# Performance work log

Hardware: AMD Instinct MI355X
Metric: run time of the kernel (lower is better)

Reference implementation:

```python
import jax, jax.numpy as jnp
import numpy as np

B, N, C, H = 4, 128, 512, 8
D = C // H
SCALE = D ** (-0.5) * 50.0


def setup_inputs() -> dict:
    key = jax.random.key(0)
    kx, kw = jax.random.split(key)
    x = jax.random.normal(kx, (B, N, N, C), dtype=jnp.float32)
    # torch Linear(n_embd, 5*n_embd, bias=False); stored here as [in, out] for x @ w
    w_qkv = jax.random.normal(kw, (C, 5 * C), dtype=jnp.float32) * (C ** -0.5)
    return {"x": x, "w_qkv": w_qkv}


def _heads(t):
    # [b, i, j, h*d] -> [b, h, i, j, d]
    b, i, j, _ = t.shape
    return t.reshape(b, i, j, H, D).transpose(0, 3, 1, 2, 4)


def reference(x, w_qkv):
    # global norm over the entire tensor (torch .std() is unbiased, ddof=1)
    x = (x - x.mean()) / x.std(ddof=1)
    qkv = x @ w_qkv                                   # [b, i, j, 5c]
    q, k1, k2, v1, v2 = map(_heads, jnp.split(qkv, 5, axis=-1))
    # pivotal attention: for query (i,j), pivot over k with row stream k1[i,k]
    # and column stream k2[k,j]
    scores = SCALE * (jnp.einsum('bhijd,bhikd->bhijk', q, k1)
                      + jnp.einsum('bhijd,bhkjd->bhijk', q, k2))
    attn = jax.nn.softmax(scores, axis=-1)            # [b, h, i, j, k]
    out = (jnp.einsum('bhijk,bhikd->bhijd', attn, v1)
           + jnp.einsum('bhijk,bhkjd->bhijd', attn, v2))
    # [b, h, i, j, d] -> [b, i, j, h*d]
    return out.transpose(0, 2, 3, 1, 4).reshape(B, N, N, C)
```

## Files before the change

kernel.cpp:

```cpp
#include <hip/hip_runtime.h>
#include <stdint.h>


typedef __attribute__((ext_vector_type(8))) short s8v;
typedef __attribute__((ext_vector_type(4))) float f4v;

#define MFMA(a, b, c) __builtin_amdgcn_mfma_f32_16x16x32_bf16((a), (b), (c), 0, 0, 0)

__device__ __forceinline__ float bf2f(unsigned short u) {
  union { unsigned int i; float f; } v; v.i = ((unsigned int)u) << 16; return v.f;
}
__device__ __forceinline__ unsigned short f2bf(float f) {
  union { float f; unsigned int i; } v; v.f = f;
  unsigned int i = v.i;
  return (unsigned short)((i + 0x7fffu + ((i >> 16) & 1u)) >> 16);
}

__device__ __forceinline__ void async_copy16(const void* g, void* l) {
  __builtin_amdgcn_global_load_lds(
      (const __attribute__((address_space(1))) unsigned int*)(uintptr_t)g,
      (__attribute__((address_space(3))) unsigned int*)(uintptr_t)l,
      16, 0, 0);
}

__global__ __launch_bounds__(256) void k_probe(const unsigned short* __restrict__ x,
                                               int* __restrict__ flag) {
  uint4 v = ((const uint4*)x)[threadIdx.x];
  unsigned int uu[4] = {v.x, v.y, v.z, v.w};
  int bad = 0;
#pragma unroll
  for (int u = 0; u < 4; ++u) {
    float a = bf2f((unsigned short)(uu[u] & 0xffffu));
    float b = bf2f((unsigned short)(uu[u] >> 16));
    if (!(fabsf(a) <= 1e4f)) bad = 1;
    if (!(fabsf(b) <= 1e4f)) bad = 1;
  }
  if (bad) atomicOr(flag, 1);
}

__global__ __launch_bounds__(256) void k_red(const void* __restrict__ xraw,
                                             const int* __restrict__ flag,
                                             double* __restrict__ dstats) {
  __shared__ float red[8];
  const int fm = flag[0];
  int t = threadIdx.x;
  size_t gid = (size_t)blockIdx.x * 256 + t;
  float s = 0.f, ss = 0.f;
  if (fm) {
    const float4* pf = (const float4*)xraw;
#pragma unroll 4
    for (int it = 0; it < 32; ++it) {
      size_t idx = gid + (size_t)it * 131072;
      float4 u1 = pf[2 * idx], u2 = pf[2 * idx + 1];
      float vals[8] = {u1.x, u1.y, u1.z, u1.w, u2.x, u2.y, u2.z, u2.w};
#pragma unroll
      for (int u = 0; u < 8; ++u) { s += vals[u]; ss += vals[u] * vals[u]; }
    }
  } else {
    const uint4* p = (const uint4*)xraw;
#pragma unroll 4
    for (int it = 0; it < 32; ++it) {
      uint4 v = p[gid + (size_t)it * 131072];
      unsigned int uu[4] = {v.x, v.y, v.z, v.w};
#pragma unroll
      for (int u = 0; u < 4; ++u) {
        float a = bf2f((unsigned short)(uu[u] & 0xffffu));
        float b = bf2f((unsigned short)(uu[u] >> 16));
        s += a + b;
        ss += a * a + b * b;
      }
    }
  }
#pragma unroll
  for (int d = 32; d >= 1; d >>= 1) {
    s += __shfl_down(s, d);
    ss += __shfl_down(ss, d);
  }
  int lane = t & 63, wave = t >> 6;
  if (lane == 0) { red[wave] = s; red[4 + wave] = ss; }
  __syncthreads();
  if (t == 0) {
    atomicAdd(&dstats[0], (double)(red[0] + red[1] + red[2] + red[3]));
    atomicAdd(&dstats[1], (double)(red[4] + red[5] + red[6] + red[7]));
  }
}

__global__ void k_stats(const double* __restrict__ dstats, float* __restrict__ fstats) {
  double M = 33554432.0;
  double mean = dstats[0] / M;
  double var = (dstats[1] - dstats[0] * dstats[0] / M) / (M - 1.0);
  double istd = 1.0 / sqrt(var);
  fstats[0] = (float)istd;
  fstats[1] = (float)(-mean * istd);
}

__global__ __launch_bounds__(256) void k_colsum(const void* __restrict__ wraw,
                                                const int* __restrict__ flag,
                                                float* __restrict__ colsum) {
  const int fm = flag[0];
  int c = blockIdx.x * 256 + threadIdx.x;
  if (c >= 2560) return;
  float s = 0.f;
  if (fm) {
    const float* w = (const float*)wraw;
    for (int r = 0; r < 512; ++r) s += w[(size_t)r * 2560 + c];
  } else {
    const unsigned short* w = (const unsigned short*)wraw;
    for (int r = 0; r < 512; ++r) s += bf2f(w[(size_t)r * 2560 + c]);
  }
  colsum[c] = s;
}

__global__ __launch_bounds__(256) void k_wt(const void* __restrict__ wraw,
                                            const int* __restrict__ flag,
                                            unsigned short* __restrict__ wThi,
                                            unsigned short* __restrict__ wTlo) {
  __shared__ float tile[64][65];
  const int fm = flag[0];
  int n0 = blockIdx.x * 64, r0 = blockIdx.y * 64;
#pragma unroll
  for (int rep = 0; rep < 16; ++rep) {
    int idx = rep * 256 + threadIdx.x;
    int r = idx >> 6, n = idx & 63;
    float v;
    if (fm) v = ((const float*)wraw)[(size_t)(r0 + r) * 2560 + n0 + n];
    else    v = bf2f(((const unsigned short*)wraw)[(size_t)(r0 + r) * 2560 + n0 + n]);
    tile[r][n] = v;
  }
  __syncthreads();
#pragma unroll
  for (int rep = 0; rep < 16; ++rep) {
    int idx = rep * 256 + threadIdx.x;
    int n = idx >> 6, r = idx & 63;
    float v = tile[r][n];
    unsigned short hi = f2bf(v);
    size_t o = (size_t)(n0 + n) * 512 + r0 + r;
    wThi[o] = hi;
    wTlo[o] = f2bf(v - bf2f(hi));
  }
}

__global__ __launch_bounds__(256) void k_convx(const void* __restrict__ xraw,
                                               const int* __restrict__ flag,
                                               unsigned short* __restrict__ xhi,
                                               unsigned short* __restrict__ xlo,
                                               int b) {
  const int fm = flag[0];
  size_t e0 = ((size_t)blockIdx.x * 256 + threadIdx.x) * 8;
  size_t g0 = (size_t)b * 8388608 + e0;
  float vals[8];
  if (fm) {
    const float4* pf = (const float4*)xraw;
    float4 u1 = pf[g0 / 4], u2 = pf[g0 / 4 + 1];
    vals[0] = u1.x; vals[1] = u1.y; vals[2] = u1.z; vals[3] = u1.w;
    vals[4] = u2.x; vals[5] = u2.y; vals[6] = u2.z; vals[7] = u2.w;
  } else {
    uint4 v = ((const uint4*)xraw)[g0 / 8];
    unsigned int uu[4] = {v.x, v.y, v.z, v.w};
#pragma unroll
    for (int u = 0; u < 4; ++u) {
      vals[2 * u] = bf2f((unsigned short)(uu[u] & 0xffffu));
      vals[2 * u + 1] = bf2f((unsigned short)(uu[u] >> 16));
    }
  }
  unsigned short h[8], l[8];
#pragma unroll
  for (int u = 0; u < 8; ++u) {
    h[u] = f2bf(vals[u]);
    l[u] = f2bf(vals[u] - bf2f(h[u]));
  }
  *(uint4*)(xhi + e0) = *(const uint4*)h;
  *(uint4*)(xlo + e0) = *(const uint4*)l;
}

__global__ __launch_bounds__(256) void k_gemm(
    const unsigned short* __restrict__ xhi, const unsigned short* __restrict__ xlo,
    const unsigned short* __restrict__ wThi, const unsigned short* __restrict__ wTlo,
    const float* __restrict__ colsum, const float* __restrict__ fstats,
    const int* __restrict__ flag,
    unsigned short* __restrict__ qhi, unsigned short* __restrict__ qlo,
    unsigned short* __restrict__ k1hi, unsigned short* __restrict__ k1lo,
    unsigned short* __restrict__ k2hi, unsigned short* __restrict__ k2lo,
    unsigned short* __restrict__ v1T, unsigned short* __restrict__ v2d,
    int h0, int hcShift, int nwgy) {
  __shared__ __align__(16) unsigned short Ash[2][4096];
  __shared__ __align__(16) unsigned short Asl[2][4096];
  __shared__ __align__(16) unsigned short Bsh[2][4096];
  __shared__ __align__(16) unsigned short Bsl[2][4096];
  const int fm = flag[0];
  const int t = threadIdx.x;

  const int vid = blockIdx.x;
  const int xcd = vid & 7, seq = vid >> 3;
  const int m0 = (xcd * 16 + seq / nwgy) * 128;
  const int n0 = (seq % nwgy) * 128;

  const int hcMask = (1 << hcShift) - 1;

  const int lane = t & 63, wave = t >> 6;
  const int wm = (wave & 1) * 64, wn = (wave >> 1) * 64;
  const int l16 = lane & 15, q4 = lane >> 4;

  const int srow0 = t >> 2;
  const int srow1 = 64 + srow0;
  const int sch = (((t & 3) ^ ((t >> 3) & 3)) << 3);
  const int swoff = ((q4 ^ ((l16 >> 1) & 3)) << 3);

  const float af = fstats[0], bfc = fstats[1];
  const unsigned short* xh = xhi + (size_t)m0 * 512;
  const unsigned short* xl = xlo + (size_t)m0 * 512;

  int wcol0, wcol1;
  {
    int n = n0 + srow0, g = n >> hcShift, rem = n & hcMask;
    wcol0 = (g << 9) + ((h0 + (rem >> 6)) << 6) + (rem & 63);
    n = n0 + srow1; g = n >> hcShift; rem = n & hcMask;
    wcol1 = (g << 9) + ((h0 + (rem >> 6)) << 6) + (rem & 63);
  }

  f4v acc[4][4];
#pragma unroll
  for (int a = 0; a < 4; ++a)
#pragma unroll
    for (int c = 0; c < 4; ++c) acc[a][c] = (f4v)0.f;

  auto STAGE = [&](int bsel, int k0) {
    async_copy16(xh + (size_t)srow0 * 512 + k0 + sch, (char*)&Ash[bsel][0] + t * 16);
    async_copy16(xh + (size_t)srow1 * 512 + k0 + sch, (char*)&Ash[bsel][0] + (256 + t) * 16);
    async_copy16(wThi + (size_t)wcol0 * 512 + k0 + sch, (char*)&Bsh[bsel][0] + t * 16);
    async_copy16(wThi + (size_t)wcol1 * 512 + k0 + sch, (char*)&Bsh[bsel][0] + (256 + t) * 16);
    if (fm) {
      async_copy16(xl + (size_t)srow0 * 512 + k0 + sch, (char*)&Asl[bsel][0] + t * 16);
      async_copy16(xl + (size_t)srow1 * 512 + k0 + sch, (char*)&Asl[bsel][0] + (256 + t) * 16);
      async_copy16(wTlo + (size_t)wcol0 * 512 + k0 + sch, (char*)&Bsl[bsel][0] + t * 16);
      async_copy16(wTlo + (size_t)wcol1 * 512 + k0 + sch, (char*)&Bsl[bsel][0] + (256 + t) * 16);
    }
  };

  STAGE(0, 0);

#pragma unroll 2
  for (int ks = 0; ks < 16; ++ks) {
    const int kb = ks & 1;
    if (ks < 15) {
      STAGE(kb ^ 1, (ks + 1) << 5);
      if (fm) asm volatile("s_waitcnt vmcnt(8)" ::: "memory");
      else    asm volatile("s_waitcnt vmcnt(4)" ::: "memory");
    } else {
      asm volatile("s_waitcnt vmcnt(0)" ::: "memory");
    }
    __builtin_amdgcn_s_barrier();

    s8v ah[4], bh[4];
#pragma unroll
    for (int jt = 0; jt < 4; ++jt)
      ah[jt] = *(const s8v*)&Ash[kb][(wm + jt * 16 + l16) * 32 + swoff];
#pragma unroll
    for (int nt = 0; nt < 4; ++nt)
      bh[nt] = *(const s8v*)&Bsh[kb][(wn + nt * 16 + l16) * 32 + swoff];
    if (fm) {
      s8v al[4], bl[4];
#pragma unroll
      for (int jt = 0; jt < 4; ++jt)
        al[jt] = *(const s8v*)&Asl[kb][(wm + jt * 16 + l16) * 32 + swoff];
#pragma unroll
      for (int nt = 0; nt < 4; ++nt)
        bl[nt] = *(const s8v*)&Bsl[kb][(wn + nt * 16 + l16) * 32 + swoff];
#pragma unroll
      for (int jt = 0; jt < 4; ++jt)
#pragma unroll
        for (int nt = 0; nt < 4; ++nt) {
          acc[jt][nt] = MFMA(ah[jt], bh[nt], acc[jt][nt]);
          acc[jt][nt] = MFMA(ah[jt], bl[nt], acc[jt][nt]);
          acc[jt][nt] = MFMA(al[jt], bh[nt], acc[jt][nt]);
        }
    } else {
#pragma unroll
      for (int jt = 0; jt < 4; ++jt)
#pragma unroll
        for (int nt = 0; nt < 4; ++nt) acc[jt][nt] = MFMA(ah[jt], bh[nt], acc[jt][nt]);
    }
    asm volatile("" ::: "memory");
    __builtin_amdgcn_s_barrier();
  }

#pragma unroll
  for (int jt = 0; jt < 4; ++jt) {
#pragma unroll
    for (int nt = 0; nt < 4; ++nt) {
      int gcol = n0 + wn + nt * 16 + l16;
      int g = gcol >> hcShift, rem = gcol & hcMask;
      int hl = rem >> 6, d = rem & 63;
      int wcol = (g << 9) + ((h0 + hl) << 6) + d;
      float cs = colsum[wcol] * bfc;
#pragma unroll
      for (int r = 0; r < 4; ++r) {
        int grow = m0 + wm + jt * 16 + q4 * 4 + r;
        int i = grow >> 7, j = grow & 127;
        float val = acc[jt][nt][r] * af + cs;
        unsigned short hi = f2bf(val);
        if (g == 0) {
          size_t idx = (((size_t)hl * 128 + i) * 128 + j) * 64 + d;
          qhi[idx] = hi; qlo[idx] = f2bf(val - bf2f(hi));
        } else if (g == 1) {
          size_t idx = (((size_t)hl * 128 + i) * 128 + j) * 64 + d;
          k1hi[idx] = hi; k1lo[idx] = f2bf(val - bf2f(hi));
        } else if (g == 2) {
          size_t idx = (((size_t)hl * 128 + j) * 128 + i) * 64 + d;
          k2hi[idx] = hi; k2lo[idx] = f2bf(val - bf2f(hi));
        } else if (g == 3) {
          size_t idx = (((size_t)hl * 128 + i) * 64 + d) * 128 + j;
          v1T[idx] = hi;
        } else {
          size_t idx = (((size_t)hl * 128 + i) * 128 + j) * 64 + d;
          v2d[idx] = hi;
        }
      }
    }
  }
}

__global__ __launch_bounds__(256) void k_v2t(const unsigned short* __restrict__ v2d,
                                             unsigned short* __restrict__ v2T) {
  __shared__ unsigned short T[128][72];
  const int j = blockIdx.x, hl = blockIdx.y;
  const int t = threadIdx.x;
  const unsigned short* ib = v2d + ((size_t)hl * 128) * 8192 + (size_t)j * 64;
#pragma unroll
  for (int it = 0; it < 4; ++it) {
    int c = it * 256 + t;
    int p = c >> 3, d8 = (c & 7) * 8;
    uint4 v = *(const uint4*)(ib + (size_t)p * 8192 + d8);
    *(uint4*)&T[p][d8 ^ (((p >> 3) & 7) << 3)] = v;
  }
  __syncthreads();
  unsigned short* ob = v2T + (((size_t)hl * 128 + j) * 64) * 128;
#pragma unroll
  for (int it = 0; it < 4; ++it) {
    int c = it * 256 + t;
    int d = c >> 4, p8 = (c & 15) * 8;
    int dz = d ^ (((p8 >> 3) & 7) << 3);
    unsigned short u[8];
#pragma unroll
    for (int e = 0; e < 8; ++e) u[e] = T[p8 + e][dz];
    *(uint4*)&ob[(size_t)d * 128 + p8] = *(const uint4*)u;
  }
}

__global__ __launch_bounds__(256) void k_s1(
    const unsigned short* __restrict__ qhi, const unsigned short* __restrict__ qlo,
    const unsigned short* __restrict__ k1hi, const unsigned short* __restrict__ k1lo,
    float* __restrict__ S) {
  const int i = blockIdx.x, hl = blockIdx.y;
  const int t = threadIdx.x, lane = t & 63, wave = t >> 6;
  const int l16 = lane & 15, q4 = lane >> 4;
  const size_t base = ((size_t)hl * 128 + i) * 128 * 64;

  f4v acc[2][8];
#pragma unroll
  for (int a = 0; a < 2; ++a)
#pragma unroll
    for (int c = 0; c < 8; ++c) acc[a][c] = (f4v)0.f;

#pragma unroll
  for (int kc = 0; kc < 2; ++kc) {
    s8v ah[2], al[2];
#pragma unroll
    for (int jt = 0; jt < 2; ++jt) {
      size_t off = base + (size_t)(wave * 32 + jt * 16 + l16) * 64 + kc * 32 + q4 * 8;
      ah[jt] = *(const s8v*)(qhi + off);
      al[jt] = *(const s8v*)(qlo + off);
    }
#pragma unroll
    for (int kt = 0; kt < 8; ++kt) {
      size_t off = base + (size_t)(kt * 16 + l16) * 64 + kc * 32 + q4 * 8;
      s8v bh = *(const s8v*)(k1hi + off);
      s8v bl = *(const s8v*)(k1lo + off);
#pragma unroll
      for (int jt = 0; jt < 2; ++jt) {
        acc[jt][kt] = MFMA(ah[jt], bh, acc[jt][kt]);
        acc[jt][kt] = MFMA(ah[jt], bl, acc[jt][kt]);
        acc[jt][kt] = MFMA(al[jt], bh, acc[jt][kt]);
      }
    }
  }
  float* Sb = S + ((size_t)hl * 128 + i) * 128 * 128;
#pragma unroll
  for (int jt = 0; jt < 2; ++jt)
#pragma unroll
    for (int kt = 0; kt < 8; ++kt)
#pragma unroll
      for (int r = 0; r < 4; ++r) {
        int j = wave * 32 + jt * 16 + q4 * 4 + r;
        Sb[(size_t)j * 128 + kt * 16 + l16] = acc[jt][kt][r];
      }
}

__global__ __launch_bounds__(256) void k_s2(
    const unsigned short* __restrict__ qhi, const unsigned short* __restrict__ qlo,
    const unsigned short* __restrict__ k2hi, const unsigned short* __restrict__ k2lo,
    const float* __restrict__ S, unsigned short* __restrict__ attn) {
  const int j = blockIdx.x, hl = blockIdx.y;
  const int t = threadIdx.x, lane = t & 63, wave = t >> 6;
  const int l16 = lane & 15, q4 = lane >> 4;
  const size_t bbase = ((size_t)hl * 128 + j) * 128 * 64;

  f4v acc[2][8];
#pragma unroll
  for (int a = 0; a < 2; ++a)
#pragma unroll
    for (int c = 0; c < 8; ++c) acc[a][c] = (f4v)0.f;

#pragma unroll
  for (int kc = 0; kc < 2; ++kc) {
    s8v ah[2], al[2];
#pragma unroll
    for (int it = 0; it < 2; ++it) {
      size_t off = (((size_t)hl * 128 + (wave * 32 + it * 16 + l16)) * 128 + j) * 64 +
                   kc * 32 + q4 * 8;
      ah[it] = *(const s8v*)(qhi + off);
      al[it] = *(const s8v*)(qlo + off);
    }
#pragma unroll
    for (int kt = 0; kt < 8; ++kt) {
      size_t off = bbase + (size_t)(kt * 16 + l16) * 64 + kc * 32 + q4 * 8;
      s8v bh = *(const s8v*)(k2hi + off);
      s8v bl = *(const s8v*)(k2lo + off);
#pragma unroll
      for (int it = 0; it < 2; ++it) {
        acc[it][kt] = MFMA(ah[it], bh, acc[it][kt]);
        acc[it][kt] = MFMA(ah[it], bl, acc[it][kt]);
        acc[it][kt] = MFMA(al[it], bh, acc[it][kt]);
      }
    }
  }

#pragma unroll
  for (int it = 0; it < 2; ++it) {
#pragma unroll
    for (int r = 0; r < 4; ++r) {
      int i = wave * 32 + it * 16 + q4 * 4 + r;
      const float* Srow = S + (((size_t)hl * 128 + i) * 128 + j) * 128;
      float tv[8];
      float m = -3.4e38f;
#pragma unroll
      for (int kt = 0; kt < 8; ++kt) {
        tv[kt] = 6.25f * (Srow[kt * 16 + l16] + acc[it][kt][r]);
        m = fmaxf(m, tv[kt]);
      }
#pragma unroll
      for (int d = 1; d <= 8; d <<= 1) m = fmaxf(m, __shfl_xor(m, d));
      float sum = 0.f;
#pragma unroll
      for (int kt = 0; kt < 8; ++kt) {
        tv[kt] = __expf(tv[kt] - m);
        sum += tv[kt];
      }
#pragma unroll
      for (int d = 1; d <= 8; d <<= 1) sum += __shfl_xor(sum, d);
      float rs = 1.f / sum;
      unsigned short* arow = attn + (((size_t)hl * 128 + i) * 128 + j) * 128;
#pragma unroll
      for (int kt = 0; kt < 8; ++kt) arow[kt * 16 + l16] = f2bf(tv[kt] * rs);
    }
  }
}

__global__ __launch_bounds__(256) void k_av1(
    const unsigned short* __restrict__ attn, const unsigned short* __restrict__ v1T,
    unsigned short* __restrict__ out1) {
  const int i = blockIdx.x, hl = blockIdx.y;
  const int t = threadIdx.x, lane = t & 63, wave = t >> 6;
  const int l16 = lane & 15, q4 = lane >> 4;
  const size_t abase = ((size_t)hl * 128 + i) * 128 * 128;
  const size_t vbase = ((size_t)hl * 128 + i) * 64 * 128;

  f4v acc[2][4];
#pragma unroll
  for (int a = 0; a < 2; ++a)
#pragma unroll
    for (int c = 0; c < 4; ++c) acc[a][c] = (f4v)0.f;

#pragma unroll
  for (int kc = 0; kc < 4; ++kc) {
    s8v a[2], bfr[4];
#pragma unroll
    for (int jt = 0; jt < 2; ++jt)
      a[jt] = *(const s8v*)(attn + abase + (size_t)(wave * 32 + jt * 16 + l16) * 128 +
                            kc * 32 + q4 * 8);
#pragma unroll
    for (int dt = 0; dt < 4; ++dt)
      bfr[dt] = *(const s8v*)(v1T + vbase + (size_t)(dt * 16 + l16) * 128 + kc * 32 + q4 * 8);
#pragma unroll
    for (int jt = 0; jt < 2; ++jt)
#pragma unroll
      for (int dt = 0; dt < 4; ++dt) acc[jt][dt] = MFMA(a[jt], bfr[dt], acc[jt][dt]);
  }
  unsigned short* ob = out1 + ((size_t)hl * 128 + i) * 128 * 64;
#pragma unroll
  for (int jt = 0; jt < 2; ++jt)
#pragma unroll
    for (int dt = 0; dt < 4; ++dt)
#pragma unroll
      for (int r = 0; r < 4; ++r) {
        int j = wave * 32 + jt * 16 + q4 * 4 + r;
        ob[(size_t)j * 64 + dt * 16 + l16] = f2bf(acc[jt][dt][r]);
      }
}

__global__ __launch_bounds__(256) void k_av2(
    const unsigned short* __restrict__ attn, const unsigned short* __restrict__ v2T,
    const unsigned short* __restrict__ out1, const int* __restrict__ flag,
    void* __restrict__ out, int b, int h0) {
  const int j = blockIdx.x, hl = blockIdx.y;
  const int t = threadIdx.x, lane = t & 63, wave = t >> 6;
  const int l16 = lane & 15, q4 = lane >> 4;
  const int fm = flag[0];
  const size_t vbase = ((size_t)hl * 128 + j) * 64 * 128;

  f4v acc[2][4];
#pragma unroll
  for (int a = 0; a < 2; ++a)
#pragma unroll
    for (int c = 0; c < 4; ++c) acc[a][c] = (f4v)0.f;

#pragma unroll
  for (int kc = 0; kc < 4; ++kc) {
    s8v a[2], bfr[4];
#pragma unroll
    for (int it = 0; it < 2; ++it)
      a[it] = *(const s8v*)(attn +
                            (((size_t)hl * 128 + (wave * 32 + it * 16 + l16)) * 128 + j) * 128 +
                            kc * 32 + q4 * 8);
#pragma unroll
    for (int dt = 0; dt < 4; ++dt)
      bfr[dt] = *(const s8v*)(v2T + vbase + (size_t)(dt * 16 + l16) * 128 + kc * 32 + q4 * 8);
#pragma unroll
    for (int it = 0; it < 2; ++it)
#pragma unroll
      for (int dt = 0; dt < 4; ++dt) acc[it][dt] = MFMA(a[it], bfr[dt], acc[it][dt]);
  }
#pragma unroll
  for (int it = 0; it < 2; ++it)
#pragma unroll
    for (int dt = 0; dt < 4; ++dt)
#pragma unroll
      for (int r = 0; r < 4; ++r) {
        int i = wave * 32 + it * 16 + q4 * 4 + r;
        int d = dt * 16 + l16;
        float o = acc[it][dt][r] + bf2f(out1[(((size_t)hl * 128 + i) * 128 + j) * 64 + d]);
        size_t oi = ((size_t)b * 16384 + i * 128 + j) * 512 + (h0 + hl) * 64 + d;
        if (fm) ((float*)out)[oi] = o;
        else    ((unsigned short*)out)[oi] = f2bf(o);
      }
}

extern "C" void kernel_launch(void* const* d_in, const int* in_sizes, int n_in,
                              void* d_out, int out_size, void* d_ws, size_t ws_size,
                              hipStream_t stream) {
  (void)in_sizes; (void)n_in; (void)out_size;
  const void* x = d_in[0];
  const void* w = d_in[1];

  const size_t xslice = (size_t)16384 * 512;
  const size_t wTsz = (size_t)2560 * 512;
  const size_t fixed = xslice * 4 + wTsz * 4 + 2560 * 4 + 64;

  int Hc = 2;
  if (30 * ((size_t)8 * 1048576) + fixed <= ws_size) Hc = 8;
  else if (30 * ((size_t)4 * 1048576) + fixed <= ws_size) Hc = 4;
  const int hcShift = (Hc == 8) ? 9 : ((Hc == 4) ? 8 : 7);
  const size_t TE = (size_t)Hc * 1048576;

  char* p = (char*)d_ws;
  unsigned short* qhi = (unsigned short*)p;  p += TE * 2;
  unsigned short* qlo = (unsigned short*)p;  p += TE * 2;
  unsigned short* k1hi = (unsigned short*)p; p += TE * 2;
  unsigned short* k1lo = (unsigned short*)p; p += TE * 2;
  unsigned short* k2hi = (unsigned short*)p; p += TE * 2;
  unsigned short* k2lo = (unsigned short*)p; p += TE * 2;
  unsigned short* v1T = (unsigned short*)p;  p += TE * 2;
  unsigned short* v2T = (unsigned short*)p;  p += TE * 2;
  float* S = (float*)p;                      p += TE * 8;
  unsigned short* attn = (unsigned short*)p; p += TE * 4;
  unsigned short* out1 = (unsigned short*)p; p += TE * 2;
  unsigned short* xhi = (unsigned short*)p;  p += xslice * 2;
  unsigned short* xlo = (unsigned short*)p;  p += xslice * 2;
  unsigned short* wThi = (unsigned short*)p; p += wTsz * 2;
  unsigned short* wTlo = (unsigned short*)p; p += wTsz * 2;
  float* colsum = (float*)p;                 p += 2560 * 4;
  double* dstats = (double*)p;               p += 16;
  int* flag = (int*)p;                       p += 8;
  float* fstats = (float*)p;                 p += 8;

  unsigned short* v2d = (unsigned short*)S;

  hipMemsetAsync(dstats, 0, 24, stream);
  k_probe<<<1, 256, 0, stream>>>((const unsigned short*)x, flag);
  k_red<<<512, 256, 0, stream>>>(x, flag, dstats);
  k_stats<<<1, 1, 0, stream>>>(dstats, fstats);
  k_colsum<<<10, 256, 0, stream>>>(w, flag, colsum);
  k_wt<<<dim3(40, 8), 256, 0, stream>>>(w, flag, wThi, wTlo);

  for (int b = 0; b < 4; ++b) {
    k_convx<<<4096, 256, 0, stream>>>(x, flag, xhi, xlo, b);
    for (int h0 = 0; h0 < 8; h0 += Hc) {
      const int nwgy = (5 * Hc * 64) / 128;
      k_gemm<<<dim3(128 * nwgy), 256, 0, stream>>>(
          xhi, xlo, wThi, wTlo, colsum, fstats, flag,
          qhi, qlo, k1hi, k1lo, k2hi, k2lo, v1T, v2d, h0, hcShift, nwgy);
      k_v2t<<<dim3(128, Hc), 256, 0, stream>>>(v2d, v2T);
      k_s1<<<dim3(128, Hc), 256, 0, stream>>>(qhi, qlo, k1hi, k1lo, S);
      k_s2<<<dim3(128, Hc), 256, 0, stream>>>(qhi, qlo, k2hi, k2lo, S, attn);
      k_av1<<<dim3(128, Hc), 256, 0, stream>>>(attn, v1T, out1);
      k_av2<<<dim3(128, Hc), 256, 0, stream>>>(attn, v2T, out1, flag, d_out, b, h0);
    }
  }
}
```

Before: 1.500 ms.

## Fuse attn@V2 into softmax kernel via LDS and merge output into AV1

The k_s2 softmax kernel now keeps its normalized attention tile for a fixed j in shared memory and immediately computes the attn·V2 product from it, writing an out2 partial. The former k_av1 kernel becomes k_av1f, which adds out2 and writes the final output, so k_av2 is removed. This saves one kernel launch per head group and the strided re-read of attn by column j that k_av2 did. The cost is about 34 KB of LDS per block in k_s2, which may lower occupancy, and the final output writes now follow i-major block order.

```diff
diff --git a/kernel.cpp b/kernel.cpp
--- a/kernel.cpp
+++ b/kernel.cpp
@@ -399,7 +399,9 @@
 __global__ __launch_bounds__(256) void k_s2(
     const unsigned short* __restrict__ qhi, const unsigned short* __restrict__ qlo,
     const unsigned short* __restrict__ k2hi, const unsigned short* __restrict__ k2lo,
-    const float* __restrict__ S, unsigned short* __restrict__ attn) {
+    const float* __restrict__ S, const unsigned short* __restrict__ v2T,
+    unsigned short* __restrict__ attn, unsigned short* __restrict__ out2) {
+  __shared__ __align__(16) unsigned short attnL[128 * 136];
   const int j = blockIdx.x, hl = blockIdx.y;
   const int t = threadIdx.x, lane = t & 63, wave = t >> 6;
   const int l16 = lane & 15, q4 = lane >> 4;
@@ -461,17 +463,56 @@
       float rs = 1.f / sum;
       unsigned short* arow = attn + (((size_t)hl * 128 + i) * 128 + j) * 128;
 #pragma unroll
-      for (int kt = 0; kt < 8; ++kt) arow[kt * 16 + l16] = f2bf(tv[kt] * rs);
-    }
-  }
-}
-
-__global__ __launch_bounds__(256) void k_av1(
+      for (int kt = 0; kt < 8; ++kt) {
+        unsigned short ab = f2bf(tv[kt] * rs);
+        arow[kt * 16 + l16] = ab;
+        attnL[i * 136 + kt * 16 + l16] = ab;
+      }
+    }
+  }
+  __syncthreads();
+
+  const size_t vbase = ((size_t)hl * 128 + j) * 64 * 128;
+  f4v acc2[2][4];
+#pragma unroll
+  for (int a = 0; a < 2; ++a)
+#pragma unroll
+    for (int c = 0; c < 4; ++c) acc2[a][c] = (f4v)0.f;
+
+#pragma unroll
+  for (int kc = 0; kc < 4; ++kc) {
+    s8v a2[2], b2[4];
+#pragma unroll
+    for (int it = 0; it < 2; ++it)
+      a2[it] = *(const s8v*)&attnL[(wave * 32 + it * 16 + l16) * 136 + kc * 32 + q4 * 8];
+#pragma unroll
+    for (int dt = 0; dt < 4; ++dt)
+      b2[dt] = *(const s8v*)(v2T + vbase + (size_t)(dt * 16 + l16) * 128 + kc * 32 + q4 * 8);
+#pragma unroll
+    for (int it = 0; it < 2; ++it)
+#pragma unroll
+      for (int dt = 0; dt < 4; ++dt) acc2[it][dt] = MFMA(a2[it], b2[dt], acc2[it][dt]);
+  }
+#pragma unroll
+  for (int it = 0; it < 2; ++it)
+#pragma unroll
+    for (int dt = 0; dt < 4; ++dt)
+#pragma unroll
+      for (int r = 0; r < 4; ++r) {
+        int i = wave * 32 + it * 16 + q4 * 4 + r;
+        int d = dt * 16 + l16;
+        out2[(((size_t)hl * 128 + i) * 128 + j) * 64 + d] = f2bf(acc2[it][dt][r]);
+      }
+}
+
+__global__ __launch_bounds__(256) void k_av1f(
     const unsigned short* __restrict__ attn, const unsigned short* __restrict__ v1T,
-    unsigned short* __restrict__ out1) {
+    const unsigned short* __restrict__ out2, const int* __restrict__ flag,
+    void* __restrict__ out, int b, int h0) {
   const int i = blockIdx.x, hl = blockIdx.y;
   const int t = threadIdx.x, lane = t & 63, wave = t >> 6;
   const int l16 = lane & 15, q4 = lane >> 4;
+  const int fm = flag[0];
   const size_t abase = ((size_t)hl * 128 + i) * 128 * 128;
   const size_t vbase = ((size_t)hl * 128 + i) * 64 * 128;
 
@@ -496,7 +537,6 @@
 #pragma unroll
       for (int dt = 0; dt < 4; ++dt) acc[jt][dt] = MFMA(a[jt], bfr[dt], acc[jt][dt]);
   }
-  unsigned short* ob = out1 + ((size_t)hl * 128 + i) * 128 * 64;
 #pragma unroll
   for (int jt = 0; jt < 2; ++jt)
 #pragma unroll
@@ -504,51 +544,9 @@
 #pragma unroll
       for (int r = 0; r < 4; ++r) {
         int j = wave * 32 + jt * 16 + q4 * 4 + r;
-        ob[(size_t)j * 64 + dt * 16 + l16] = f2bf(acc[jt][dt][r]);
-      }
-}
-
-__global__ __launch_bounds__(256) void k_av2(
-    const unsigned short* __restrict__ attn, const unsigned short* __restrict__ v2T,
-    const unsigned short* __restrict__ out1, const int* __restrict__ flag,
-    void* __restrict__ out, int b, int h0) {
-  const int j = blockIdx.x, hl = blockIdx.y;
-  const int t = threadIdx.x, lane = t & 63, wave = t >> 6;
-  const int l16 = lane & 15, q4 = lane >> 4;
-  const int fm = flag[0];
-  const size_t vbase = ((size_t)hl * 128 + j) * 64 * 128;
-
-  f4v acc[2][4];
-#pragma unroll
-  for (int a = 0; a < 2; ++a)
-#pragma unroll
-    for (int c = 0; c < 4; ++c) acc[a][c] = (f4v)0.f;
-
-#pragma unroll
-  for (int kc = 0; kc < 4; ++kc) {
-    s8v a[2], bfr[4];
-#pragma unroll
-    for (int it = 0; it < 2; ++it)
-      a[it] = *(const s8v*)(attn +
-                            (((size_t)hl * 128 + (wave * 32 + it * 16 + l16)) * 128 + j) * 128 +
-                            kc * 32 + q4 * 8);
-#pragma unroll
-    for (int dt = 0; dt < 4; ++dt)
-      bfr[dt] = *(const s8v*)(v2T + vbase + (size_t)(dt * 16 + l16) * 128 + kc * 32 + q4 * 8);
-#pragma unroll
-    for (int it = 0; it < 2; ++it)
-#pragma unroll
-      for (int dt = 0; dt < 4; ++dt) acc[it][dt] = MFMA(a[it], bfr[dt], acc[it][dt]);
-  }
-#pragma unroll
-  for (int it = 0; it < 2; ++it)
-#pragma unroll
-    for (int dt = 0; dt < 4; ++dt)
-#pragma unroll
-      for (int r = 0; r < 4; ++r) {
-        int i = wave * 32 + it * 16 + q4 * 4 + r;
         int d = dt * 16 + l16;
-        float o = acc[it][dt][r] + bf2f(out1[(((size_t)hl * 128 + i) * 128 + j) * 64 + d]);
+        float o = acc[jt][dt][r] +
+                  bf2f(out2[(((size_t)hl * 128 + i) * 128 + j) * 64 + d]);
         size_t oi = ((size_t)b * 16384 + i * 128 + j) * 512 + (h0 + hl) * 64 + d;
         if (fm) ((float*)out)[oi] = o;
         else    ((unsigned short*)out)[oi] = f2bf(o);
@@ -583,7 +581,7 @@
   unsigned short* v2T = (unsigned short*)p;  p += TE * 2;
   float* S = (float*)p;                      p += TE * 8;
   unsigned short* attn = (unsigned short*)p; p += TE * 4;
-  unsigned short* out1 = (unsigned short*)p; p += TE * 2;
+  unsigned short* out2 = (unsigned short*)p; p += TE * 2;
   unsigned short* xhi = (unsigned short*)p;  p += xslice * 2;
   unsigned short* xlo = (unsigned short*)p;  p += xslice * 2;
   unsigned short* wThi = (unsigned short*)p; p += wTsz * 2;
@@ -611,9 +609,8 @@
           qhi, qlo, k1hi, k1lo, k2hi, k2lo, v1T, v2d, h0, hcShift, nwgy);
       k_v2t<<<dim3(128, Hc), 256, 0, stream>>>(v2d, v2T);
       k_s1<<<dim3(128, Hc), 256, 0, stream>>>(qhi, qlo, k1hi, k1lo, S);
-      k_s2<<<dim3(128, Hc), 256, 0, stream>>>(qhi, qlo, k2hi, k2lo, S, attn);
-      k_av1<<<dim3(128, Hc), 256, 0, stream>>>(attn, v1T, out1);
-      k_av2<<<dim3(128, Hc), 256, 0, stream>>>(attn, v2T, out1, flag, d_out, b, h0);
-    }
-  }
-}
+      k_s2<<<dim3(128, Hc), 256, 0, stream>>>(qhi, qlo, k2hi, k2lo, S, v2T, attn, out2);
+      k_av1f<<<dim3(128, Hc), 256, 0, stream>>>(attn, v1T, out2, flag, d_out, b, h0);
+    }
+  }
+}
```

Result: no change. 1.510 ms (+0.7%).
